# Optimization experiments

Hardware: AMD Instinct MI355X
Metric: run time of the kernel (lower is better)

The kernel has to match this reference:

```python
import jax, jax.numpy as jnp
import numpy as np

N = 100000   # num_embeddings
D = 128      # embedding_dims
E = 128      # edge_output_size
S = 2048     # number of streaming interactions
W_DECAY = 1.0  # Decayer w, decay_method='exp': f(dt) = exp(-w*dt)


def setup_inputs() -> dict:
    key = jax.random.key(0)
    ks = jax.random.split(key, 20)
    def nrm(k, shape, s):
        return jax.random.normal(k, shape, jnp.float32) * s
    sD = 1.0 / np.sqrt(D)
    sE = 1.0 / np.sqrt(E)
    return {
        'heads': jax.random.randint(ks[0], (S,), 0, N, dtype=jnp.int32),
        'tails': jax.random.randint(ks[1], (S,), 0, N, dtype=jnp.int32),
        'times': jnp.sort(jax.random.uniform(ks[2], (S,), jnp.float32) * 100.0),
        # node state tables (nn.Embedding weights in the original)
        'node_rep': nrm(ks[3], (N, D), 0.1),
        'cell_head': nrm(ks[4], (N, D), 0.1),
        'hidden_head': nrm(ks[5], (N, D), 0.1),
        'cell_tail': nrm(ks[6], (N, D), 0.1),
        'hidden_tail': nrm(ks[7], (N, D), 0.1),
        # Edge_updater_nn head / tail: act(rep_h @ W1 + rep_t @ W2 + b)
        'Weh1': nrm(ks[8], (D, E), sD), 'Weh2': nrm(ks[9], (D, E), sD), 'beh': jnp.zeros((E,), jnp.float32),
        'Wet1': nrm(ks[10], (D, E), sD), 'Wet2': nrm(ks[11], (D, E), sD), 'bet': jnp.zeros((E,), jnp.float32),
        # TLSTM head (time-decayed LSTM cell)
        'Wxh': nrm(ks[12], (E, 4 * D), sE), 'Whh': nrm(ks[13], (D, 4 * D), sD), 'bh': jnp.zeros((4 * D,), jnp.float32),
        'Wdh': nrm(ks[14], (D, D), sD), 'bdh': jnp.zeros((D,), jnp.float32),
        # TLSTM tail
        'Wxt': nrm(ks[15], (E, 4 * D), sE), 'Wht': nrm(ks[16], (D, 4 * D), sD), 'bt': jnp.zeros((4 * D,), jnp.float32),
        'Wdt': nrm(ks[17], (D, D), sD), 'bdt': jnp.zeros((D,), jnp.float32),
        # Combiner: tanh(h_head @ Wc1 + h_tail @ Wc2)
        'Wc1': nrm(ks[18], (D, D), sD), 'Wc2': nrm(ks[19], (D, D), sD),
    }


def _tlstm(x, c, h, decay, Wx, Wh, b, Wd, bd):
    # Time-aware LSTM: decompose short-term memory, decay it by elapsed time, recombine.
    cs = jnp.tanh(c @ Wd + bd)      # short-term memory component
    c_adj = c - cs + cs * decay      # adjusted previous cell
    z = x @ Wx + h @ Wh + b          # [4D] gate pre-activations
    i, f, o, g = jnp.split(z, 4)
    i = jax.nn.sigmoid(i); f = jax.nn.sigmoid(f); o = jax.nn.sigmoid(o)
    g = jnp.tanh(g)
    c_new = f * c_adj + i * g
    h_new = o * jnp.tanh(c_new)
    return c_new, h_new


def reference(heads, tails, times, node_rep, cell_head, hidden_head, cell_tail, hidden_tail,
              Weh1, Weh2, beh, Wet1, Wet2, bet,
              Wxh, Whh, bh, Wdh, bdh, Wxt, Wht, bt, Wdt, bdt, Wc1, Wc2):
    recent = jnp.zeros((node_rep.shape[0],), jnp.float32)  # recent_timestamp, init 0

    def step(state, ev):
        rep, ch, hh, ct, ht, rt = state
        h_i, t_i, tm = ev
        rep_h = rep[h_i]                    # gather current reps
        rep_t = rep[t_i]
        dec_h = jnp.exp(-W_DECAY * (tm - rt[h_i]))   # decayer(delta_t)
        dec_t = jnp.exp(-W_DECAY * (tm - rt[t_i]))
        edge_h = jnp.tanh(rep_h @ Weh1 + rep_t @ Weh2 + beh)  # edge_updater_head
        edge_t = jnp.tanh(rep_h @ Wet1 + rep_t @ Wet2 + bet)  # edge_updater_tail
        c_h, h_h = _tlstm(edge_h, ch[h_i], hh[h_i], dec_h, Wxh, Whh, bh, Wdh, bdh)
        c_t, h_t = _tlstm(edge_t, ct[t_i], ht[t_i], dec_t, Wxt, Wht, bt, Wdt, bdt)
        new_rep_h = jnp.tanh(h_h @ Wc1 + ht[h_i] @ Wc2)  # combiner(head hidden, tail hidden)
        new_rep_t = jnp.tanh(hh[t_i] @ Wc1 + h_t @ Wc2)
        # scatter updated state (head written before tail, matching original ordering)
        rep = rep.at[h_i].set(new_rep_h).at[t_i].set(new_rep_t)
        ch = ch.at[h_i].set(c_h); hh = hh.at[h_i].set(h_h)
        ct = ct.at[t_i].set(c_t); ht = ht.at[t_i].set(h_t)
        rt = rt.at[h_i].set(tm).at[t_i].set(tm)
        # if_updated=0: emit pre-update representations for this interaction
        return (rep, ch, hh, ct, ht, rt), (rep_h, rep_t)

    state0 = (node_rep, cell_head, hidden_head, cell_tail, hidden_tail, recent)
    _, (out_h, out_t) = jax.lax.scan(step, state0, (heads, tails, times))
    return jnp.stack([out_h, out_t])  # [2, S, D]
```

## Files before the change

kernel.cpp:

```cpp
#include <hip/hip_runtime.h>
#include <hip/hip_cooperative_groups.h>
#include <math.h>

namespace cg = cooperative_groups;

#define NBLK_MAX 1024
#define DD 128
#define SMAX 2048

__device__ __forceinline__ float sigmoidf(float x) { return 1.0f / (1.0f + expf(-x)); }

__global__ __launch_bounds__(64) void pred_kernel(
    const int* __restrict__ heads, const int* __restrict__ tails, int S,
    int* __restrict__ ph, int* __restrict__ pt) {
  const int j = blockIdx.x;
  if (j >= S) return;
  const int myh = heads[j], myt = tails[j];
  const int lane = threadIdx.x;
  int mph = -1, mpt = -1;
  for (int i = lane; i < j; i += 64) {
    int a = heads[i], b = tails[i];
    if (a == myh || b == myh) mph = i;
    if (a == myt || b == myt) mpt = i;
  }
#pragma unroll
  for (int off = 32; off > 0; off >>= 1) {
    mph = max(mph, __shfl_down(mph, off));
    mpt = max(mpt, __shfl_down(mpt, off));
  }
  if (lane == 0) { ph[j] = mph; pt[j] = mpt; }
}

__global__ __launch_bounds__(1024) void finalize_kernel(
    int S, const int* __restrict__ phg, const int* __restrict__ ptg,
    int* __restrict__ order, int* __restrict__ level_off, int* __restrict__ n_levels) {
  __shared__ int lvl[SMAX], ph[SMAX], pt[SMAX], cnt[SMAX];
  __shared__ int changed, maxl;
  const int tid = threadIdx.x;

  for (int j = tid; j < S; j += 1024) { ph[j] = phg[j]; pt[j] = ptg[j]; lvl[j] = 1; }
  __syncthreads();

  for (int it = 0; it < S + 2; ++it) {
    if (tid == 0) changed = 0;
    __syncthreads();
    for (int j = tid; j < S; j += 1024) {
      int l = 1;
      int a = ph[j]; if (a >= 0) l = lvl[a] + 1;
      int b = pt[j]; if (b >= 0) { int lb = lvl[b] + 1; if (lb > l) l = lb; }
      if (l != lvl[j]) { lvl[j] = l; changed = 1; }
    }
    __syncthreads();
    if (!changed) break;
    __syncthreads();
  }

  if (tid == 0) maxl = 0;
  __syncthreads();
  for (int j = tid; j < S; j += 1024) atomicMax(&maxl, lvl[j]);
  __syncthreads();
  const int M = maxl;

  for (int l = tid; l < M; l += 1024) cnt[l] = 0;
  __syncthreads();
  for (int j = tid; j < S; j += 1024) atomicAdd(&cnt[lvl[j] - 1], 1);
  __syncthreads();
  if (tid == 0) {
    int run = 0;
    level_off[0] = 0;
    for (int l = 0; l < M; ++l) { run += cnt[l]; level_off[l + 1] = run; }
    n_levels[0] = M;
  }
  __syncthreads();

  for (int l = tid; l < M; l += 1024) cnt[l] = 0;
  __syncthreads();
  for (int j = tid; j < S; j += 1024) {
    int lv = lvl[j] - 1;
    int pos = level_off[lv] + atomicAdd(&cnt[lv], 1);
    order[pos] = j;
  }
}

struct PParams {
  const int* heads; const int* tails; const float* times;
  float* node_rep; float* cell_head; float* hidden_head; float* cell_tail; float* hidden_tail;
  const float* Weh1; const float* Weh2; const float* beh;
  const float* Wet1; const float* Wet2; const float* bet;
  const float* Wxh; const float* Whh; const float* bh; const float* Wdh; const float* bdh;
  const float* Wxt; const float* Wht; const float* bt; const float* Wdt; const float* bdt;
  const float* Wc1; const float* Wc2;
  float* out; float* rt;
  const int* order; const int* level_off; const int* n_levels;
  int S;
};

__global__ __launch_bounds__(256) void process_kernel(PParams p) {
  cg::grid_group grid = cg::this_grid();
  const int tid = threadIdx.x;

  __shared__ float repH[DD], repT[DD], cHs[DD], hHs[DD], cTs[DD], hTs[DD];
  __shared__ float htH[DD], hhT[DD];
  __shared__ float edgeH[DD], edgeT[DD], cadjH[DD], cadjT[DD];
  __shared__ float zH[512], zT[512];
  __shared__ float nhH[DD], nhT[DD];
  __shared__ float dec2[2], tmS;
  __shared__ int idx2[2];

  int nlv = p.n_levels[0];
  if (nlv < 0) nlv = 0;
  if (nlv > SMAX) nlv = SMAX;
  for (int lv = 0; lv < nlv; ++lv) {
    const int beg = p.level_off[lv], end = p.level_off[lv + 1];
    for (int k = beg + blockIdx.x; k < end; k += gridDim.x) {
      __syncthreads();
      const int s = p.order[k];
      if (tid == 0) { idx2[0] = p.heads[s]; idx2[1] = p.tails[s]; tmS = p.times[s]; }
      __syncthreads();
      const int hI = idx2[0], tI = idx2[1];
      const float tm = tmS;
      if (tid < 2) dec2[tid] = expf(-(tm - p.rt[idx2[tid]]));

      if (tid < DD) {
        const int d = tid;
        const size_t o = (size_t)hI * DD + d;
        float r = p.node_rep[o];
        repH[d] = r; cHs[d] = p.cell_head[o]; hHs[d] = p.hidden_head[o];
        htH[d] = p.hidden_tail[o];
        p.out[(size_t)s * DD + d] = r;
      } else {
        const int d = tid - DD;
        const size_t o = (size_t)tI * DD + d;
        float r = p.node_rep[o];
        repT[d] = r; cTs[d] = p.cell_tail[o]; hTs[d] = p.hidden_tail[o];
        hhT[d] = p.hidden_head[o];
        p.out[(size_t)(p.S + s) * DD + d] = r;
      }
      __syncthreads();

      if (tid < DD) {
        const int e = tid;
        float ae = p.beh[e], ac = p.bdh[e];
#pragma unroll 4
        for (int d = 0; d < DD; ++d) {
          ae += repH[d] * p.Weh1[d * DD + e] + repT[d] * p.Weh2[d * DD + e];
          ac += cHs[d] * p.Wdh[d * DD + e];
        }
        edgeH[e] = tanhf(ae);
        float cs = tanhf(ac);
        cadjH[e] = cHs[e] - cs + cs * dec2[0];
      } else {
        const int e = tid - DD;
        float ae = p.bet[e], ac = p.bdt[e];
#pragma unroll 4
        for (int d = 0; d < DD; ++d) {
          ae += repH[d] * p.Wet1[d * DD + e] + repT[d] * p.Wet2[d * DD + e];
          ac += cTs[d] * p.Wdt[d * DD + e];
        }
        edgeT[e] = tanhf(ae);
        float cs = tanhf(ac);
        cadjT[e] = cTs[e] - cs + cs * dec2[1];
      }
      __syncthreads();

      {
        float a0 = p.bh[tid], a1 = p.bh[tid + 256];
        float b0 = p.bt[tid], b1 = p.bt[tid + 256];
#pragma unroll 2
        for (int d = 0; d < DD; ++d) {
          const float eh = edgeH[d], hh = hHs[d], et = edgeT[d], ht = hTs[d];
          a0 += eh * p.Wxh[d * 512 + tid]       + hh * p.Whh[d * 512 + tid];
          a1 += eh * p.Wxh[d * 512 + tid + 256] + hh * p.Whh[d * 512 + tid + 256];
          b0 += et * p.Wxt[d * 512 + tid]       + ht * p.Wht[d * 512 + tid];
          b1 += et * p.Wxt[d * 512 + tid + 256] + ht * p.Wht[d * 512 + tid + 256];
        }
        zH[tid] = a0; zH[tid + 256] = a1;
        zT[tid] = b0; zT[tid + 256] = b1;
      }
      __syncthreads();

      if (tid < DD) {
        const int e = tid;
        float ig = sigmoidf(zH[e]), fg = sigmoidf(zH[DD + e]);
        float og = sigmoidf(zH[256 + e]), gg = tanhf(zH[384 + e]);
        float c = fg * cadjH[e] + ig * gg;
        float h = og * tanhf(c);
        nhH[e] = h;
        p.cell_head[(size_t)hI * DD + e] = c;
        p.hidden_head[(size_t)hI * DD + e] = h;
      } else {
        const int e = tid - DD;
        float ig = sigmoidf(zT[e]), fg = sigmoidf(zT[DD + e]);
        float og = sigmoidf(zT[256 + e]), gg = tanhf(zT[384 + e]);
        float c = fg * cadjT[e] + ig * gg;
        float h = og * tanhf(c);
        nhT[e] = h;
        p.cell_tail[(size_t)tI * DD + e] = c;
        p.hidden_tail[(size_t)tI * DD + e] = h;
      }
      if (tid == 0) p.rt[hI] = tm;
      if (tid == 1) p.rt[tI] = tm;
      __syncthreads();

      if (tid < DD) {
        const int e = tid;
        float a = 0.f;
#pragma unroll 4
        for (int d = 0; d < DD; ++d)
          a += nhH[d] * p.Wc1[d * DD + e] + htH[d] * p.Wc2[d * DD + e];
        if (hI != tI) p.node_rep[(size_t)hI * DD + e] = tanhf(a);
      } else {
        const int e = tid - DD;
        float a = 0.f;
#pragma unroll 4
        for (int d = 0; d < DD; ++d)
          a += hhT[d] * p.Wc1[d * DD + e] + nhT[d] * p.Wc2[d * DD + e];
        p.node_rep[(size_t)tI * DD + e] = tanhf(a);
      }
    }
    __threadfence();
    grid.sync();
  }
}

extern "C" void kernel_launch(void* const* d_in, const int* in_sizes, int n_in,
                              void* d_out, int out_size, void* d_ws, size_t ws_size,
                              hipStream_t stream) {
  const int* heads = (const int*)d_in[0];
  const int* tails = (const int*)d_in[1];
  const float* times = (const float*)d_in[2];
  float* node_rep    = (float*)d_in[3];
  float* cell_head   = (float*)d_in[4];
  float* hidden_head = (float*)d_in[5];
  float* cell_tail   = (float*)d_in[6];
  float* hidden_tail = (float*)d_in[7];
  const float* Weh1 = (const float*)d_in[8];
  const float* Weh2 = (const float*)d_in[9];
  const float* beh  = (const float*)d_in[10];
  const float* Wet1 = (const float*)d_in[11];
  const float* Wet2 = (const float*)d_in[12];
  const float* bet  = (const float*)d_in[13];
  const float* Wxh  = (const float*)d_in[14];
  const float* Whh  = (const float*)d_in[15];
  const float* bh   = (const float*)d_in[16];
  const float* Wdh  = (const float*)d_in[17];
  const float* bdh  = (const float*)d_in[18];
  const float* Wxt  = (const float*)d_in[19];
  const float* Wht  = (const float*)d_in[20];
  const float* bt   = (const float*)d_in[21];
  const float* Wdt  = (const float*)d_in[22];
  const float* bdt  = (const float*)d_in[23];
  const float* Wc1  = (const float*)d_in[24];
  const float* Wc2  = (const float*)d_in[25];

  const int S = in_sizes[0];
  const int N = in_sizes[3] / DD;

  char* ws = (char*)d_ws;
  float* rt = (float*)ws;
  size_t rtBytes = (((size_t)N * 4) + 511) & ~(size_t)511;
  int* order     = (int*)(ws + rtBytes);
  int* level_off = order + SMAX;
  int* n_levels  = level_off + SMAX + 1;
  int* ph        = n_levels + 64;
  int* pt        = ph + SMAX;

  hipMemsetAsync(rt, 0, (size_t)N * 4, stream);
  pred_kernel<<<S, 64, 0, stream>>>(heads, tails, S, ph, pt);
  finalize_kernel<<<1, 1024, 0, stream>>>(S, ph, pt, order, level_off, n_levels);

  PParams p;
  p.heads = heads; p.tails = tails; p.times = times;
  p.node_rep = node_rep; p.cell_head = cell_head; p.hidden_head = hidden_head;
  p.cell_tail = cell_tail; p.hidden_tail = hidden_tail;
  p.Weh1 = Weh1; p.Weh2 = Weh2; p.beh = beh;
  p.Wet1 = Wet1; p.Wet2 = Wet2; p.bet = bet;
  p.Wxh = Wxh; p.Whh = Whh; p.bh = bh; p.Wdh = Wdh; p.bdh = bdh;
  p.Wxt = Wxt; p.Wht = Wht; p.bt = bt; p.Wdt = Wdt; p.bdt = bdt;
  p.Wc1 = Wc1; p.Wc2 = Wc2;
  p.out = (float*)d_out; p.rt = rt;
  p.order = order; p.level_off = level_off; p.n_levels = n_levels;
  p.S = S;

  void* args[] = { (void*)&p };

  int dev = 0; hipGetDevice(&dev);
  int nCU = 0;
  hipDeviceGetAttribute(&nCU, hipDeviceAttributeMultiprocessorCount, dev);
  if (nCU <= 0) nCU = 256;
  int maxBlkPerCU = 0;
  hipOccupancyMaxActiveBlocksPerMultiprocessor(&maxBlkPerCU, process_kernel, 256, 0);
  if (maxBlkPerCU < 1) maxBlkPerCU = 1;
  long long cap = (long long)nCU * (long long)maxBlkPerCU;
  int grid = (int)(cap < NBLK_MAX ? cap : NBLK_MAX);
  if (grid < 1) grid = nCU;

  hipError_t err = hipLaunchCooperativeKernel(process_kernel, dim3(grid), dim3(256),
                                              args, 0, stream);
  if (err != hipSuccess && grid > 512) {
    err = hipLaunchCooperativeKernel(process_kernel, dim3(512), dim3(256), args, 0, stream);
  }
  if (err != hipSuccess && grid > 256) {
    err = hipLaunchCooperativeKernel(process_kernel, dim3(256), dim3(256), args, 0, stream);
  }
}
```

Before: 779.0 us.

## Batch up to four interactions per block to reuse weight loads

Each block now handles up to G=4 independent interactions of a level at once. Per-interaction vectors are stored interleaved in shared memory, so every weight element read from global memory feeds four accumulators. Blocks grow to 512 threads and the grid cap drops to 512, and the work for each matmul stage is redistributed across thread roles. The aim is to cut per-interaction weight traffic and barrier overhead; the cost is less parallelism across blocks when a level holds only a few interactions.

```diff
diff --git a/kernel.cpp b/kernel.cpp
--- a/kernel.cpp
+++ b/kernel.cpp
@@ -4,8 +4,10 @@
 
 namespace cg = cooperative_groups;
 
-#define NBLK_MAX 1024
 #define DD 128
+#define G 4
+#define TPB 512
+#define NBLK_MAX 512
 #define SMAX 2048
 
 __device__ __forceinline__ float sigmoidf(float x) { return 1.0f / (1.0f + expf(-x)); }
@@ -95,127 +97,200 @@
   int S;
 };
 
-__global__ __launch_bounds__(256) void process_kernel(PParams p) {
+__global__ __launch_bounds__(TPB) void process_kernel(PParams p) {
   cg::grid_group grid = cg::this_grid();
   const int tid = threadIdx.x;
 
-  __shared__ float repH[DD], repT[DD], cHs[DD], hHs[DD], cTs[DD], hTs[DD];
-  __shared__ float htH[DD], hhT[DD];
-  __shared__ float edgeH[DD], edgeT[DD], cadjH[DD], cadjT[DD];
-  __shared__ float zH[512], zT[512];
-  __shared__ float nhH[DD], nhT[DD];
-  __shared__ float dec2[2], tmS;
-  __shared__ int idx2[2];
+  __shared__ __align__(16) float S_[12288];
+  __shared__ int sIdx[G], hIdx[G], tIdx[G];
+  __shared__ float tmv[G], decHs[G], decTs[G];
+
+  const int O_REPH = 0,    O_REPT = 1024, O_CHS = 2048, O_CTS = 3072;
+  const int O_ZH   = 0,    O_ZT   = 2048;
+  const int O_HHS  = 4096, O_HTS  = 5120, O_HTH = 6144, O_HHT = 7168;
+  const int O_EH   = 8192, O_ET   = 9216;
+  const int O_CAH  = 10240, O_CAT = 11264;
 
   int nlv = p.n_levels[0];
   if (nlv < 0) nlv = 0;
   if (nlv > SMAX) nlv = SMAX;
+
   for (int lv = 0; lv < nlv; ++lv) {
     const int beg = p.level_off[lv], end = p.level_off[lv + 1];
-    for (int k = beg + blockIdx.x; k < end; k += gridDim.x) {
-      __syncthreads();
-      const int s = p.order[k];
-      if (tid == 0) { idx2[0] = p.heads[s]; idx2[1] = p.tails[s]; tmS = p.times[s]; }
-      __syncthreads();
-      const int hI = idx2[0], tI = idx2[1];
-      const float tm = tmS;
-      if (tid < 2) dec2[tid] = expf(-(tm - p.rt[idx2[tid]]));
-
-      if (tid < DD) {
-        const int d = tid;
-        const size_t o = (size_t)hI * DD + d;
-        float r = p.node_rep[o];
-        repH[d] = r; cHs[d] = p.cell_head[o]; hHs[d] = p.hidden_head[o];
-        htH[d] = p.hidden_tail[o];
-        p.out[(size_t)s * DD + d] = r;
-      } else {
-        const int d = tid - DD;
-        const size_t o = (size_t)tI * DD + d;
-        float r = p.node_rep[o];
-        repT[d] = r; cTs[d] = p.cell_tail[o]; hTs[d] = p.hidden_tail[o];
-        hhT[d] = p.hidden_head[o];
-        p.out[(size_t)(p.S + s) * DD + d] = r;
-      }
-      __syncthreads();
-
-      if (tid < DD) {
-        const int e = tid;
-        float ae = p.beh[e], ac = p.bdh[e];
-#pragma unroll 4
+    const int Lsz = end - beg;
+    int gE = (Lsz + (int)gridDim.x - 1) / (int)gridDim.x;
+    if (gE > G) gE = G;
+    if (gE < 1) gE = 1;
+
+    for (int base = beg + (int)blockIdx.x * gE; base < end; base += (int)gridDim.x * gE) {
+      const int ng = min(gE, end - base);
+      __syncthreads();
+      if (tid < ng) {
+        int s = p.order[base + tid]; sIdx[tid] = s;
+        int h = p.heads[s], t = p.tails[s];
+        hIdx[tid] = h; tIdx[tid] = t;
+        float tm = p.times[s]; tmv[tid] = tm;
+        decHs[tid] = expf(-(tm - p.rt[h]));
+        decTs[tid] = expf(-(tm - p.rt[t]));
+      }
+      __syncthreads();
+
+      {
+        const int g = tid >> 7, d = tid & 127;
+        if (g < ng) {
+          const size_t oh = (size_t)hIdx[g] * DD + d;
+          const size_t ot = (size_t)tIdx[g] * DD + d;
+          const int b = d * 8 + g;
+          float rh = p.node_rep[oh];
+          S_[O_REPH + b] = rh; p.out[(size_t)sIdx[g] * DD + d] = rh;
+          S_[O_CHS + b] = p.cell_head[oh];
+          S_[O_HHS + b] = p.hidden_head[oh];
+          S_[O_HTH + b] = p.hidden_tail[oh];
+          float rt_ = p.node_rep[ot];
+          S_[O_REPT + b] = rt_; p.out[(size_t)(p.S + sIdx[g]) * DD + d] = rt_;
+          S_[O_CTS + b] = p.cell_tail[ot];
+          S_[O_HTS + b] = p.hidden_tail[ot];
+          S_[O_HHT + b] = p.hidden_head[ot];
+        }
+      }
+      __syncthreads();
+
+      {
+        const int role = tid >> 7, e = tid & 127;
+        if (role == 0) {
+          float a0 = p.beh[e], a1 = a0, a2 = a0, a3 = a0;
+          for (int d = 0; d < DD; ++d) {
+            float w1 = p.Weh1[d * DD + e], w2 = p.Weh2[d * DD + e];
+            float4 rh = *(const float4*)&S_[O_REPH + d * 8];
+            float4 rt4 = *(const float4*)&S_[O_REPT + d * 8];
+            a0 += rh.x * w1 + rt4.x * w2; a1 += rh.y * w1 + rt4.y * w2;
+            a2 += rh.z * w1 + rt4.z * w2; a3 += rh.w * w1 + rt4.w * w2;
+          }
+          float4 o; o.x = tanhf(a0); o.y = tanhf(a1); o.z = tanhf(a2); o.w = tanhf(a3);
+          *(float4*)&S_[O_EH + e * 8] = o;
+        } else if (role == 1) {
+          float a0 = p.bet[e], a1 = a0, a2 = a0, a3 = a0;
+          for (int d = 0; d < DD; ++d) {
+            float w1 = p.Wet1[d * DD + e], w2 = p.Wet2[d * DD + e];
+            float4 rh = *(const float4*)&S_[O_REPH + d * 8];
+            float4 rt4 = *(const float4*)&S_[O_REPT + d * 8];
+            a0 += rh.x * w1 + rt4.x * w2; a1 += rh.y * w1 + rt4.y * w2;
+            a2 += rh.z * w1 + rt4.z * w2; a3 += rh.w * w1 + rt4.w * w2;
+          }
+          float4 o; o.x = tanhf(a0); o.y = tanhf(a1); o.z = tanhf(a2); o.w = tanhf(a3);
+          *(float4*)&S_[O_ET + e * 8] = o;
+        } else if (role == 2) {
+          float a0 = p.bdh[e], a1 = a0, a2 = a0, a3 = a0;
+          for (int d = 0; d < DD; ++d) {
+            float wd = p.Wdh[d * DD + e];
+            float4 c4 = *(const float4*)&S_[O_CHS + d * 8];
+            a0 += c4.x * wd; a1 += c4.y * wd; a2 += c4.z * wd; a3 += c4.w * wd;
+          }
+          float cs0 = tanhf(a0), cs1 = tanhf(a1), cs2 = tanhf(a2), cs3 = tanhf(a3);
+          float4 o;
+          o.x = S_[O_CHS + e * 8 + 0] - cs0 + cs0 * decHs[0];
+          o.y = S_[O_CHS + e * 8 + 1] - cs1 + cs1 * decHs[1];
+          o.z = S_[O_CHS + e * 8 + 2] - cs2 + cs2 * decHs[2];
+          o.w = S_[O_CHS + e * 8 + 3] - cs3 + cs3 * decHs[3];
+          *(float4*)&S_[O_CAH + e * 8] = o;
+        } else {
+          float a0 = p.bdt[e], a1 = a0, a2 = a0, a3 = a0;
+          for (int d = 0; d < DD; ++d) {
+            float wd = p.Wdt[d * DD + e];
+            float4 c4 = *(const float4*)&S_[O_CTS + d * 8];
+            a0 += c4.x * wd; a1 += c4.y * wd; a2 += c4.z * wd; a3 += c4.w * wd;
+          }
+          float cs0 = tanhf(a0), cs1 = tanhf(a1), cs2 = tanhf(a2), cs3 = tanhf(a3);
+          float4 o;
+          o.x = S_[O_CTS + e * 8 + 0] - cs0 + cs0 * decTs[0];
+          o.y = S_[O_CTS + e * 8 + 1] - cs1 + cs1 * decTs[1];
+          o.z = S_[O_CTS + e * 8 + 2] - cs2 + cs2 * decTs[2];
+          o.w = S_[O_CTS + e * 8 + 3] - cs3 + cs3 * decTs[3];
+          *(float4*)&S_[O_CAT + e * 8] = o;
+        }
+      }
+      __syncthreads();
+
+      {
+        const int c = tid;
+        float h0 = p.bh[c], h1 = h0, h2 = h0, h3 = h0;
+        float t0 = p.bt[c], t1 = t0, t2 = t0, t3 = t0;
         for (int d = 0; d < DD; ++d) {
-          ae += repH[d] * p.Weh1[d * DD + e] + repT[d] * p.Weh2[d * DD + e];
-          ac += cHs[d] * p.Wdh[d * DD + e];
-        }
-        edgeH[e] = tanhf(ae);
-        float cs = tanhf(ac);
-        cadjH[e] = cHs[e] - cs + cs * dec2[0];
-      } else {
-        const int e = tid - DD;
-        float ae = p.bet[e], ac = p.bdt[e];
-#pragma unroll 4
-        for (int d = 0; d < DD; ++d) {
-          ae += repH[d] * p.Wet1[d * DD + e] + repT[d] * p.Wet2[d * DD + e];
-          ac += cTs[d] * p.Wdt[d * DD + e];
-        }
-        edgeT[e] = tanhf(ae);
-        float cs = tanhf(ac);
-        cadjT[e] = cTs[e] - cs + cs * dec2[1];
-      }
-      __syncthreads();
-
-      {
-        float a0 = p.bh[tid], a1 = p.bh[tid + 256];
-        float b0 = p.bt[tid], b1 = p.bt[tid + 256];
-#pragma unroll 2
-        for (int d = 0; d < DD; ++d) {
-          const float eh = edgeH[d], hh = hHs[d], et = edgeT[d], ht = hTs[d];
-          a0 += eh * p.Wxh[d * 512 + tid]       + hh * p.Whh[d * 512 + tid];
-          a1 += eh * p.Wxh[d * 512 + tid + 256] + hh * p.Whh[d * 512 + tid + 256];
-          b0 += et * p.Wxt[d * 512 + tid]       + ht * p.Wht[d * 512 + tid];
-          b1 += et * p.Wxt[d * 512 + tid + 256] + ht * p.Wht[d * 512 + tid + 256];
-        }
-        zH[tid] = a0; zH[tid + 256] = a1;
-        zT[tid] = b0; zT[tid + 256] = b1;
-      }
-      __syncthreads();
-
-      if (tid < DD) {
-        const int e = tid;
-        float ig = sigmoidf(zH[e]), fg = sigmoidf(zH[DD + e]);
-        float og = sigmoidf(zH[256 + e]), gg = tanhf(zH[384 + e]);
-        float c = fg * cadjH[e] + ig * gg;
-        float h = og * tanhf(c);
-        nhH[e] = h;
-        p.cell_head[(size_t)hI * DD + e] = c;
-        p.hidden_head[(size_t)hI * DD + e] = h;
-      } else {
-        const int e = tid - DD;
-        float ig = sigmoidf(zT[e]), fg = sigmoidf(zT[DD + e]);
-        float og = sigmoidf(zT[256 + e]), gg = tanhf(zT[384 + e]);
-        float c = fg * cadjT[e] + ig * gg;
-        float h = og * tanhf(c);
-        nhT[e] = h;
-        p.cell_tail[(size_t)tI * DD + e] = c;
-        p.hidden_tail[(size_t)tI * DD + e] = h;
-      }
-      if (tid == 0) p.rt[hI] = tm;
-      if (tid == 1) p.rt[tI] = tm;
-      __syncthreads();
-
-      if (tid < DD) {
-        const int e = tid;
-        float a = 0.f;
-#pragma unroll 4
-        for (int d = 0; d < DD; ++d)
-          a += nhH[d] * p.Wc1[d * DD + e] + htH[d] * p.Wc2[d * DD + e];
-        if (hI != tI) p.node_rep[(size_t)hI * DD + e] = tanhf(a);
-      } else {
-        const int e = tid - DD;
-        float a = 0.f;
-#pragma unroll 4
-        for (int d = 0; d < DD; ++d)
-          a += hhT[d] * p.Wc1[d * DD + e] + nhT[d] * p.Wc2[d * DD + e];
-        p.node_rep[(size_t)tI * DD + e] = tanhf(a);
+          float wxh = p.Wxh[d * 512 + c], whh = p.Whh[d * 512 + c];
+          float wxt = p.Wxt[d * 512 + c], wht = p.Wht[d * 512 + c];
+          float4 ex = *(const float4*)&S_[O_EH + d * 8];
+          float4 hx = *(const float4*)&S_[O_HHS + d * 8];
+          float4 et = *(const float4*)&S_[O_ET + d * 8];
+          float4 ht4 = *(const float4*)&S_[O_HTS + d * 8];
+          h0 += ex.x * wxh + hx.x * whh; h1 += ex.y * wxh + hx.y * whh;
+          h2 += ex.z * wxh + hx.z * whh; h3 += ex.w * wxh + hx.w * whh;
+          t0 += et.x * wxt + ht4.x * wht; t1 += et.y * wxt + ht4.y * wht;
+          t2 += et.z * wxt + ht4.z * wht; t3 += et.w * wxt + ht4.w * wht;
+        }
+        float4 zh; zh.x = h0; zh.y = h1; zh.z = h2; zh.w = h3;
+        float4 zt; zt.x = t0; zt.y = t1; zt.z = t2; zt.w = t3;
+        *(float4*)&S_[O_ZH + c * 4] = zh;
+        *(float4*)&S_[O_ZT + c * 4] = zt;
+      }
+      __syncthreads();
+
+      {
+        const int side = tid >> 8, sub = (tid >> 7) & 1, e = tid & 127;
+        const int zo = side ? O_ZT : O_ZH;
+        const int co = side ? O_CAT : O_CAH;
+        const int no = side ? O_ET : O_EH;
+        float* ctab = side ? p.cell_tail : p.cell_head;
+        float* htab = side ? p.hidden_tail : p.hidden_head;
+        for (int q = 0; q < 2; ++q) {
+          int g = sub + 2 * q;
+          if (g >= ng) continue;
+          float iv = sigmoidf(S_[zo + e * 4 + g]);
+          float fv = sigmoidf(S_[zo + (128 + e) * 4 + g]);
+          float ov = sigmoidf(S_[zo + (256 + e) * 4 + g]);
+          float gv = tanhf(S_[zo + (384 + e) * 4 + g]);
+          float cadj = S_[co + e * 8 + g];
+          float cn = fv * cadj + iv * gv;
+          float hn = ov * tanhf(cn);
+          S_[no + e * 8 + g] = hn;
+          int node = side ? tIdx[g] : hIdx[g];
+          ctab[(size_t)node * DD + e] = cn;
+          htab[(size_t)node * DD + e] = hn;
+        }
+        if (tid < 2 * G) {
+          int g = tid & (G - 1);
+          if (g < ng) p.rt[(tid >= G) ? tIdx[g] : hIdx[g]] = tmv[g];
+        }
+      }
+      __syncthreads();
+
+      {
+        const int role = tid >> 7, e = tid & 127;
+        if (role == 0) {
+          float a0 = 0.f, a1 = 0.f, a2 = 0.f, a3 = 0.f;
+          for (int d = 0; d < DD; ++d) {
+            float w1 = p.Wc1[d * DD + e], w2 = p.Wc2[d * DD + e];
+            float4 x = *(const float4*)&S_[O_EH + d * 8];
+            float4 y = *(const float4*)&S_[O_HTH + d * 8];
+            a0 += x.x * w1 + y.x * w2; a1 += x.y * w1 + y.y * w2;
+            a2 += x.z * w1 + y.z * w2; a3 += x.w * w1 + y.w * w2;
+          }
+          float r[4] = {a0, a1, a2, a3};
+          for (int g = 0; g < ng; ++g)
+            if (hIdx[g] != tIdx[g])
+              p.node_rep[(size_t)hIdx[g] * DD + e] = tanhf(r[g]);
+        } else if (role == 1) {
+          float a0 = 0.f, a1 = 0.f, a2 = 0.f, a3 = 0.f;
+          for (int d = 0; d < DD; ++d) {
+            float w1 = p.Wc1[d * DD + e], w2 = p.Wc2[d * DD + e];
+            float4 x = *(const float4*)&S_[O_HHT + d * 8];
+            float4 y = *(const float4*)&S_[O_ET + d * 8];
+            a0 += x.x * w1 + y.x * w2; a1 += x.y * w1 + y.y * w2;
+            a2 += x.z * w1 + y.z * w2; a3 += x.w * w1 + y.w * w2;
+          }
+          float r[4] = {a0, a1, a2, a3};
+          for (int g = 0; g < ng; ++g)
+            p.node_rep[(size_t)tIdx[g] * DD + e] = tanhf(r[g]);
+        }
       }
     }
     __threadfence();
@@ -289,18 +364,18 @@
   hipDeviceGetAttribute(&nCU, hipDeviceAttributeMultiprocessorCount, dev);
   if (nCU <= 0) nCU = 256;
   int maxBlkPerCU = 0;
-  hipOccupancyMaxActiveBlocksPerMultiprocessor(&maxBlkPerCU, process_kernel, 256, 0);
+  hipOccupancyMaxActiveBlocksPerMultiprocessor(&maxBlkPerCU, process_kernel, TPB, 0);
   if (maxBlkPerCU < 1) maxBlkPerCU = 1;
   long long cap = (long long)nCU * (long long)maxBlkPerCU;
   int grid = (int)(cap < NBLK_MAX ? cap : NBLK_MAX);
   if (grid < 1) grid = nCU;
 
-  hipError_t err = hipLaunchCooperativeKernel(process_kernel, dim3(grid), dim3(256),
+  hipError_t err = hipLaunchCooperativeKernel(process_kernel, dim3(grid), dim3(TPB),
                                               args, 0, stream);
-  if (err != hipSuccess && grid > 512) {
-    err = hipLaunchCooperativeKernel(process_kernel, dim3(512), dim3(256), args, 0, stream);
-  }
   if (err != hipSuccess && grid > 256) {
-    err = hipLaunchCooperativeKernel(process_kernel, dim3(256), dim3(256), args, 0, stream);
+    err = hipLaunchCooperativeKernel(process_kernel, dim3(256), dim3(TPB), args, 0, stream);
+  }
+  if (err != hipSuccess && grid > 128) {
+    err = hipLaunchCooperativeKernel(process_kernel, dim3(128), dim3(TPB), args, 0, stream);
   }
 }
```

Result: slower. 795.5 us (+2.1%).
